# Kernel tuning notes

Hardware: AMD Instinct MI355X
Metric: run time of the kernel (lower is better)

The kernel has to match this reference:

```python
import jax, jax.numpy as jnp
import numpy as np

B, S, D, H = 2, 1024, 1024, 16
DH = D // H
EPS = 1e-5

def _ln(x, g, b):
    m = jnp.mean(x, axis=-1, keepdims=True)
    v = jnp.mean((x - m) ** 2, axis=-1, keepdims=True)
    return (x - m) / jnp.sqrt(v + EPS) * g + b

def setup_inputs() -> dict:
    key = jax.random.key(0)
    ks = jax.random.split(key, 5)
    scale = 1.0 / np.sqrt(D)
    return {
        "id": jax.random.normal(ks[0], (B, S, D), dtype=jnp.float32),
        "Wq": jax.random.uniform(ks[1], (D, D), jnp.float32, -scale, scale),
        "Wk": jax.random.uniform(ks[2], (D, D), jnp.float32, -scale, scale),
        "Wv": jax.random.uniform(ks[3], (D, D), jnp.float32, -scale, scale),
        "g0": jnp.ones((D,), jnp.float32), "b0": jnp.zeros((D,), jnp.float32),
        "g1": jnp.ones((D,), jnp.float32), "b1": jnp.zeros((D,), jnp.float32),
        "g2": jnp.ones((D,), jnp.float32), "b2": jnp.zeros((D,), jnp.float32),
    }

def reference(id, Wq, Wk, Wv, g0, b0, g1, b1, g2, b2):
    residual = id
    id_ln = _ln(id, g0, b0)
    # torch Linear: x @ W.T ; split heads along last dim, cat along batch
    q = (id_ln @ Wq.T).reshape(B, S, H, DH)
    k = (id_ln @ Wk.T).reshape(B, S, H, DH)
    v = (id_ln @ Wv.T).reshape(B, S, H, DH)
    scores = jnp.einsum('bqhd,bkhd->bhqk', q, k) / np.sqrt(DH)
    A = jax.nn.softmax(scores, axis=-1)                      # [B,H,S,S]
    O = jnp.einsum('bhqk,bkhd->bqhd', A, v).reshape(B, S, D)  # merge heads
    left = _ln(id_ln + O, g1, b1)
    right = _ln(residual + O, g2, b2)
    out = left + right
    # torch layout of A is [(H*B), S, S] with head-major ordering
    A_out = jnp.transpose(A, (1, 0, 2, 3)).reshape(H * B, S, S)
    return (out, A_out)
```

## Files before the change

### kernel.cpp

```cpp
#include <hip/hip_runtime.h>

namespace {

constexpr int B = 2, S = 1024, D = 1024, H = 16, DH = 64;
constexpr int M = B * S;
constexpr float EPS = 1e-5f;

using bf16x8 = __attribute__((ext_vector_type(8))) short;
using f32x4  = __attribute__((ext_vector_type(4))) float;

typedef const __attribute__((address_space(1))) void* gptr_t;
typedef __attribute__((address_space(3))) void* lptr_t;

__device__ __forceinline__ unsigned short f2bf(float f) {
    union { float f; unsigned u; } v{f};
    unsigned r = v.u + 0x7fffu + ((v.u >> 16) & 1u);
    return (unsigned short)(r >> 16);
}

__device__ __forceinline__ float wave_sum(float v) {
#pragma unroll
    for (int off = 32; off > 0; off >>= 1) v += __shfl_down(v, off, 64);
    return v;
}

__global__ __launch_bounds__(256) void cvt_w_kernel(
    const float* __restrict__ Wq, const float* __restrict__ Wk,
    const float* __restrict__ Wv, unsigned short* __restrict__ Wb)
{
    const float* src = (blockIdx.z == 0) ? Wq : (blockIdx.z == 1) ? Wk : Wv;
    const size_t i = ((size_t)blockIdx.x * 256 + threadIdx.x) * 4;
    float4 f = *reinterpret_cast<const float4*>(src + i);
    ushort4 h;
    h.x = f2bf(f.x); h.y = f2bf(f.y); h.z = f2bf(f.z); h.w = f2bf(f.w);
    *reinterpret_cast<ushort4*>(Wb + (size_t)blockIdx.z * D * D + i) = h;
}

__global__ __launch_bounds__(256) void ln0_kernel(
    const float* __restrict__ x, const float* __restrict__ g,
    const float* __restrict__ bt, float* __restrict__ y,
    unsigned short* __restrict__ yb)
{
    __shared__ float sm[8];
    __shared__ float stats[2];
    const int row = blockIdx.x;
    const int t = threadIdx.x;
    const float4 v = reinterpret_cast<const float4*>(x + (size_t)row * D)[t];
    float s  = v.x + v.y + v.z + v.w;
    float ss = v.x*v.x + v.y*v.y + v.z*v.z + v.w*v.w;
    s = wave_sum(s); ss = wave_sum(ss);
    const int lane = t & 63, wid = t >> 6;
    if (lane == 0) { sm[wid] = s; sm[4 + wid] = ss; }
    __syncthreads();
    if (t == 0) {
        float S1 = sm[0] + sm[1] + sm[2] + sm[3];
        float S2 = sm[4] + sm[5] + sm[6] + sm[7];
        float m  = S1 * (1.0f / D);
        float var = S2 * (1.0f / D) - m * m;
        stats[0] = m; stats[1] = rsqrtf(var + EPS);
    }
    __syncthreads();
    const float m = stats[0], r = stats[1];
    const float4 gv = reinterpret_cast<const float4*>(g)[t];
    const float4 bv = reinterpret_cast<const float4*>(bt)[t];
    float4 o;
    o.x = (v.x - m) * r * gv.x + bv.x;
    o.y = (v.y - m) * r * gv.y + bv.y;
    o.z = (v.z - m) * r * gv.z + bv.z;
    o.w = (v.w - m) * r * gv.w + bv.w;
    reinterpret_cast<float4*>(y + (size_t)row * D)[t] = o;
    ushort4 h; h.x = f2bf(o.x); h.y = f2bf(o.y); h.z = f2bf(o.z); h.w = f2bf(o.w);
    *reinterpret_cast<ushort4*>(yb + (size_t)row * D + t * 4) = h;
}

__global__ __launch_bounds__(256) void qkv_mfma_kernel(
    const unsigned short* __restrict__ idln, const unsigned short* __restrict__ Wb,
    unsigned short* __restrict__ q, unsigned short* __restrict__ k,
    unsigned short* __restrict__ vT)
{
    __shared__ unsigned short As[128 * 32];
    __shared__ unsigned short Bs[128 * 32];
    const int zi = blockIdx.z;
    const unsigned short* Bmat = Wb + (size_t)zi * D * D;
    const int m0 = blockIdx.y * 128, n0 = blockIdx.x * 128;
    const int t = threadIdx.x;
    const int w = t >> 6, lane = t & 63;
    const int wm = (w >> 1) * 64, wn = (w & 1) * 64;
    const int quad = lane >> 4, l16 = lane & 15;
    const int srow = t >> 2;
    const int scol = (t & 3) * 8;

    f32x4 acc[4][4];
#pragma unroll
    for (int i = 0; i < 4; ++i)
#pragma unroll
        for (int j = 0; j < 4; ++j) acc[i][j] = (f32x4){0.f, 0.f, 0.f, 0.f};

    for (int k0 = 0; k0 < D; k0 += 32) {
        __syncthreads();
#pragma unroll
        for (int c = 0; c < 2; ++c) {
            const unsigned short* ga = idln + (size_t)(m0 + srow + c * 64) * D + k0 + scol;
            __builtin_amdgcn_global_load_lds((gptr_t)ga, (lptr_t)(As + t * 8 + c * 2048), 16, 0, 0);
            const unsigned short* gb = Bmat + (size_t)(n0 + srow + c * 64) * D + k0 + scol;
            __builtin_amdgcn_global_load_lds((gptr_t)gb, (lptr_t)(Bs + t * 8 + c * 2048), 16, 0, 0);
        }
        __syncthreads();
        bf16x8 af[4], bfr[4];
#pragma unroll
        for (int i = 0; i < 4; ++i)
            af[i] = *reinterpret_cast<const bf16x8*>(As + (wm + i * 16 + l16) * 32 + quad * 8);
#pragma unroll
        for (int j = 0; j < 4; ++j)
            bfr[j] = *reinterpret_cast<const bf16x8*>(Bs + (wn + j * 16 + l16) * 32 + quad * 8);
#pragma unroll
        for (int i = 0; i < 4; ++i)
#pragma unroll
            for (int j = 0; j < 4; ++j)
                acc[i][j] = __builtin_amdgcn_mfma_f32_16x16x32_bf16(af[i], bfr[j], acc[i][j], 0, 0, 0);
    }

    if (zi < 2) {
        unsigned short* C = (zi == 0) ? q : k;
#pragma unroll
        for (int i = 0; i < 4; ++i)
#pragma unroll
            for (int j = 0; j < 4; ++j) {
                const int gcol = n0 + wn + j * 16 + l16;
#pragma unroll
                for (int reg = 0; reg < 4; ++reg) {
                    const int grow = m0 + wm + i * 16 + quad * 4 + reg;
                    C[(size_t)grow * D + gcol] = f2bf(acc[i][j][reg]);
                }
            }
    } else {
        const int b = m0 >> 10;
#pragma unroll
        for (int i = 0; i < 4; ++i)
#pragma unroll
            for (int j = 0; j < 4; ++j) {
                const int gcol = n0 + wn + j * 16 + l16;
                const int srow0 = (m0 - b * S) + wm + i * 16 + quad * 4;
                ushort4 h;
                h.x = f2bf(acc[i][j][0]); h.y = f2bf(acc[i][j][1]);
                h.z = f2bf(acc[i][j][2]); h.w = f2bf(acc[i][j][3]);
                *reinterpret_cast<ushort4*>(vT + ((size_t)b * D + gcol) * S + srow0) = h;
            }
    }
}

__global__ __launch_bounds__(256) void attn_fused_kernel(
    const unsigned short* __restrict__ q, const unsigned short* __restrict__ k,
    const unsigned short* __restrict__ vT, float* __restrict__ Aout,
    float* __restrict__ O)
{
    __shared__ unsigned short Qs[2 * 64 * 32];
    __shared__ unsigned short Ks[2 * 128 * 32];
    __shared__ unsigned short Vs[4 * 64 * 32];
    __shared__ unsigned short Ps[4 * 64 * 32];
    __shared__ float rs[4][64];
    __shared__ float sInv[64];

    const int z = blockIdx.z;
    const int b = z & 1, h = z >> 1;
    const int m0 = blockIdx.y * 64;
    const int t = threadIdx.x;
    const int w = t >> 6, lane = t & 63;
    const int quad = lane >> 4, l16 = lane & 15;
    const int wn = w * 32;
    const int sr = t >> 2, sc8 = (t & 3) * 8;

#pragma unroll
    for (int c = 0; c < 2; ++c) {
        const unsigned short* gq = q + (size_t)(b * S + m0 + sr) * D + h * DH + c * 32 + sc8;
        __builtin_amdgcn_global_load_lds((gptr_t)gq, (lptr_t)(Qs + c * 2048 + t * 8), 16, 0, 0);
    }

    float part[4][4];
#pragma unroll
    for (int i = 0; i < 4; ++i)
#pragma unroll
        for (int r = 0; r < 4; ++r) part[i][r] = 0.f;

    for (int n0 = 0; n0 < S; n0 += 128) {
        __syncthreads();
#pragma unroll
        for (int c = 0; c < 2; ++c)
#pragma unroll
            for (int cc = 0; cc < 2; ++cc) {
                const unsigned short* gk = k + (size_t)(b * S + n0 + cc * 64 + sr) * D + h * DH + c * 32 + sc8;
                __builtin_amdgcn_global_load_lds((gptr_t)gk, (lptr_t)(Ks + c * 4096 + cc * 2048 + t * 8), 16, 0, 0);
            }
        __syncthreads();
        f32x4 acc[4][2];
#pragma unroll
        for (int i = 0; i < 4; ++i)
#pragma unroll
            for (int j = 0; j < 2; ++j) acc[i][j] = (f32x4){0.f, 0.f, 0.f, 0.f};
#pragma unroll
        for (int c = 0; c < 2; ++c) {
            bf16x8 af[4], bfr[2];
#pragma unroll
            for (int i = 0; i < 4; ++i)
                af[i] = *reinterpret_cast<const bf16x8*>(Qs + c * 2048 + (i * 16 + l16) * 32 + quad * 8);
#pragma unroll
            for (int j = 0; j < 2; ++j)
                bfr[j] = *reinterpret_cast<const bf16x8*>(Ks + c * 4096 + (wn + j * 16 + l16) * 32 + quad * 8);
#pragma unroll
            for (int i = 0; i < 4; ++i)
#pragma unroll
                for (int j = 0; j < 2; ++j)
                    acc[i][j] = __builtin_amdgcn_mfma_f32_16x16x32_bf16(af[i], bfr[j], acc[i][j], 0, 0, 0);
        }
#pragma unroll
        for (int i = 0; i < 4; ++i)
#pragma unroll
            for (int j = 0; j < 2; ++j)
#pragma unroll
                for (int r = 0; r < 4; ++r)
                    part[i][r] += __expf(acc[i][j][r] * 0.125f);
    }
#pragma unroll
    for (int i = 0; i < 4; ++i)
#pragma unroll
        for (int r = 0; r < 4; ++r) {
            float p = part[i][r];
#pragma unroll
            for (int off = 1; off < 16; off <<= 1) p += __shfl_xor(p, off, 64);
            if (l16 == 0) rs[w][i * 16 + quad * 4 + r] = p;
        }
    __syncthreads();
    if (t < 64) sInv[t] = 1.0f / (rs[0][t] + rs[1][t] + rs[2][t] + rs[3][t]);

    float* Az = Aout + (size_t)z * S * S;
    f32x4 accO[4];
#pragma unroll
    for (int j = 0; j < 4; ++j) accO[j] = (f32x4){0.f, 0.f, 0.f, 0.f};

    for (int n0 = 0; n0 < S; n0 += 128) {
        __syncthreads();
#pragma unroll
        for (int c = 0; c < 2; ++c)
#pragma unroll
            for (int cc = 0; cc < 2; ++cc) {
                const unsigned short* gk = k + (size_t)(b * S + n0 + cc * 64 + sr) * D + h * DH + c * 32 + sc8;
                __builtin_amdgcn_global_load_lds((gptr_t)gk, (lptr_t)(Ks + c * 4096 + cc * 2048 + t * 8), 16, 0, 0);
            }
#pragma unroll
        for (int ks = 0; ks < 4; ++ks) {
            const unsigned short* gv = vT + ((size_t)b * D + h * DH + sr) * S + n0 + ks * 32 + sc8;
            __builtin_amdgcn_global_load_lds((gptr_t)gv, (lptr_t)(Vs + ks * 2048 + t * 8), 16, 0, 0);
        }
        __syncthreads();
        f32x4 acc[4][2];
#pragma unroll
        for (int i = 0; i < 4; ++i)
#pragma unroll
            for (int j = 0; j < 2; ++j) acc[i][j] = (f32x4){0.f, 0.f, 0.f, 0.f};
#pragma unroll
        for (int c = 0; c < 2; ++c) {
            bf16x8 af[4], bfr[2];
#pragma unroll
            for (int i = 0; i < 4; ++i)
                af[i] = *reinterpret_cast<const bf16x8*>(Qs + c * 2048 + (i * 16 + l16) * 32 + quad * 8);
#pragma unroll
            for (int j = 0; j < 2; ++j)
                bfr[j] = *reinterpret_cast<const bf16x8*>(Ks + c * 4096 + (wn + j * 16 + l16) * 32 + quad * 8);
#pragma unroll
            for (int i = 0; i < 4; ++i)
#pragma unroll
                for (int j = 0; j < 2; ++j)
                    acc[i][j] = __builtin_amdgcn_mfma_f32_16x16x32_bf16(af[i], bfr[j], acc[i][j], 0, 0, 0);
        }
#pragma unroll
        for (int i = 0; i < 4; ++i)
#pragma unroll
            for (int j = 0; j < 2; ++j)
#pragma unroll
                for (int r = 0; r < 4; ++r) {
                    const int rl = i * 16 + quad * 4 + r;
                    float a = __expf(acc[i][j][r] * 0.125f) * sInv[rl];
                    Az[(size_t)(m0 + rl) * S + n0 + wn + j * 16 + l16] = a;
                    Ps[w * 2048 + rl * 32 + j * 16 + l16] = f2bf(a);
                }
        __syncthreads();
#pragma unroll
        for (int ks = 0; ks < 4; ++ks) {
            bf16x8 af = *reinterpret_cast<const bf16x8*>(Ps + ks * 2048 + (w * 16 + l16) * 32 + quad * 8);
#pragma unroll
            for (int j = 0; j < 4; ++j) {
                bf16x8 bfr = *reinterpret_cast<const bf16x8*>(Vs + ks * 2048 + (j * 16 + l16) * 32 + quad * 8);
                accO[j] = __builtin_amdgcn_mfma_f32_16x16x32_bf16(af, bfr, accO[j], 0, 0, 0);
            }
        }
    }
#pragma unroll
    for (int j = 0; j < 4; ++j)
#pragma unroll
        for (int r = 0; r < 4; ++r) {
            const int grow = b * S + m0 + w * 16 + quad * 4 + r;
            O[(size_t)grow * D + h * DH + j * 16 + l16] = accO[j][r];
        }
}

__global__ __launch_bounds__(256) void final_kernel(
    const float* __restrict__ id, const float* __restrict__ id_ln, const float* __restrict__ O,
    const float* __restrict__ g1, const float* __restrict__ b1,
    const float* __restrict__ g2, const float* __restrict__ b2,
    float* __restrict__ out)
{
    __shared__ float sm[16];
    __shared__ float stats[4];
    const int row = blockIdx.x;
    const int t = threadIdx.x;
    const size_t base = (size_t)row * D;
    const float4 xi = reinterpret_cast<const float4*>(id + base)[t];
    const float4 xl = reinterpret_cast<const float4*>(id_ln + base)[t];
    const float4 xo = reinterpret_cast<const float4*>(O + base)[t];
    float4 t1, t2;
    t1.x = xl.x + xo.x; t1.y = xl.y + xo.y; t1.z = xl.z + xo.z; t1.w = xl.w + xo.w;
    t2.x = xi.x + xo.x; t2.y = xi.y + xo.y; t2.z = xi.z + xo.z; t2.w = xi.w + xo.w;
    float s1  = t1.x + t1.y + t1.z + t1.w;
    float ss1 = t1.x*t1.x + t1.y*t1.y + t1.z*t1.z + t1.w*t1.w;
    float s2  = t2.x + t2.y + t2.z + t2.w;
    float ss2 = t2.x*t2.x + t2.y*t2.y + t2.z*t2.z + t2.w*t2.w;
    s1 = wave_sum(s1); ss1 = wave_sum(ss1);
    s2 = wave_sum(s2); ss2 = wave_sum(ss2);
    const int lane = t & 63, wid = t >> 6;
    if (lane == 0) { sm[wid] = s1; sm[4+wid] = ss1; sm[8+wid] = s2; sm[12+wid] = ss2; }
    __syncthreads();
    if (t == 0) {
        float S1 = sm[0]+sm[1]+sm[2]+sm[3];
        float Q1 = sm[4]+sm[5]+sm[6]+sm[7];
        float S2 = sm[8]+sm[9]+sm[10]+sm[11];
        float Q2 = sm[12]+sm[13]+sm[14]+sm[15];
        float m1 = S1 * (1.0f / D);
        float m2 = S2 * (1.0f / D);
        stats[0] = m1; stats[1] = rsqrtf(Q1 * (1.0f / D) - m1*m1 + EPS);
        stats[2] = m2; stats[3] = rsqrtf(Q2 * (1.0f / D) - m2*m2 + EPS);
    }
    __syncthreads();
    const float m1 = stats[0], r1 = stats[1], m2 = stats[2], r2 = stats[3];
    const float4 g1v = reinterpret_cast<const float4*>(g1)[t];
    const float4 b1v = reinterpret_cast<const float4*>(b1)[t];
    const float4 g2v = reinterpret_cast<const float4*>(g2)[t];
    const float4 b2v = reinterpret_cast<const float4*>(b2)[t];
    float4 o;
    o.x = (t1.x - m1)*r1*g1v.x + b1v.x + (t2.x - m2)*r2*g2v.x + b2v.x;
    o.y = (t1.y - m1)*r1*g1v.y + b1v.y + (t2.y - m2)*r2*g2v.y + b2v.y;
    o.z = (t1.z - m1)*r1*g1v.z + b1v.z + (t2.z - m2)*r2*g2v.z + b2v.z;
    o.w = (t1.w - m1)*r1*g1v.w + b1v.w + (t2.w - m2)*r2*g2v.w + b2v.w;
    reinterpret_cast<float4*>(out + base)[t] = o;
}

}

extern "C" void kernel_launch(void* const* d_in, const int* in_sizes, int n_in,
                              void* d_out, int out_size, void* d_ws, size_t ws_size,
                              hipStream_t stream)
{
    const float* id = (const float*)d_in[0];
    const float* Wq = (const float*)d_in[1];
    const float* Wk = (const float*)d_in[2];
    const float* Wv = (const float*)d_in[3];
    const float* g0 = (const float*)d_in[4];
    const float* b0 = (const float*)d_in[5];
    const float* g1 = (const float*)d_in[6];
    const float* b1 = (const float*)d_in[7];
    const float* g2 = (const float*)d_in[8];
    const float* b2 = (const float*)d_in[9];

    float* out  = (float*)d_out;
    float* Aout = out + (size_t)B * S * D;

    char* ws = (char*)d_ws;
    float* id_ln  = (float*)(ws);
    float* O      = (float*)(ws + (8u << 20));
    unsigned short* idln_bf = (unsigned short*)(ws + (16u << 20));
    unsigned short* Wb      = idln_bf + (size_t)M * D;
    unsigned short* qb      = Wb + (size_t)3 * D * D;
    unsigned short* kb      = qb + (size_t)M * D;
    unsigned short* vT      = kb + (size_t)M * D;

    hipLaunchKernelGGL(cvt_w_kernel, dim3(D * D / 1024, 1, 3), dim3(256), 0, stream,
                       Wq, Wk, Wv, Wb);
    hipLaunchKernelGGL(ln0_kernel, dim3(M), dim3(256), 0, stream, id, g0, b0, id_ln, idln_bf);
    hipLaunchKernelGGL(qkv_mfma_kernel, dim3(D / 128, M / 128, 3), dim3(256), 0, stream,
                       idln_bf, Wb, qb, kb, vT);
    hipLaunchKernelGGL(attn_fused_kernel, dim3(1, S / 64, H * B), dim3(256), 0, stream,
                       qb, kb, vT, Aout, O);
    hipLaunchKernelGGL(final_kernel, dim3(M), dim3(256), 0, stream,
                       id, id_ln, O, g1, b1, g2, b2, out);
}
```

Baseline: 233.3 us.

## Restructure attention so each wave owns query rows and keeps P in registers

The attention kernel now has each wave own 16 query rows. It computes S^T via MFMA with K as the A operand, so the row sums stay in-lane and no cross-wave LDS reduction is needed. The probabilities feed the PV MFMA (16x16x16) straight from registers instead of going through a shared-memory P buffer, which removes a barrier per tile. A is now written as float4 vector stores, and the K/V tiles are narrowed to 64 keys per tile. In exchange there are more loop iterations with two barriers each, and it relies on the smaller-K bf16 MFMA.

```diff
diff --git a/kernel.cpp b/kernel.cpp
--- a/kernel.cpp
+++ b/kernel.cpp
@@ -7,6 +7,7 @@
 constexpr float EPS = 1e-5f;
 
 using bf16x8 = __attribute__((ext_vector_type(8))) short;
+using bf16x4 = __attribute__((ext_vector_type(4))) short;
 using f32x4  = __attribute__((ext_vector_type(4))) float;
 
 typedef const __attribute__((address_space(1))) void* gptr_t;
@@ -155,10 +156,8 @@
     float* __restrict__ O)
 {
     __shared__ unsigned short Qs[2 * 64 * 32];
-    __shared__ unsigned short Ks[2 * 128 * 32];
-    __shared__ unsigned short Vs[4 * 64 * 32];
-    __shared__ unsigned short Ps[4 * 64 * 32];
-    __shared__ float rs[4][64];
+    __shared__ unsigned short Ks[2 * 64 * 32];
+    __shared__ unsigned short Vs[4 * 64 * 16];
     __shared__ float sInv[64];
 
     const int z = blockIdx.z;
@@ -167,7 +166,6 @@
     const int t = threadIdx.x;
     const int w = t >> 6, lane = t & 63;
     const int quad = lane >> 4, l16 = lane & 15;
-    const int wn = w * 32;
     const int sr = t >> 2, sc8 = (t & 3) * 8;
 
 #pragma unroll
@@ -175,131 +173,89 @@
         const unsigned short* gq = q + (size_t)(b * S + m0 + sr) * D + h * DH + c * 32 + sc8;
         __builtin_amdgcn_global_load_lds((gptr_t)gq, (lptr_t)(Qs + c * 2048 + t * 8), 16, 0, 0);
     }
-
-    float part[4][4];
-#pragma unroll
-    for (int i = 0; i < 4; ++i)
-#pragma unroll
-        for (int r = 0; r < 4; ++r) part[i][r] = 0.f;
-
-    for (int n0 = 0; n0 < S; n0 += 128) {
-        __syncthreads();
-#pragma unroll
-        for (int c = 0; c < 2; ++c)
-#pragma unroll
-            for (int cc = 0; cc < 2; ++cc) {
-                const unsigned short* gk = k + (size_t)(b * S + n0 + cc * 64 + sr) * D + h * DH + c * 32 + sc8;
-                __builtin_amdgcn_global_load_lds((gptr_t)gk, (lptr_t)(Ks + c * 4096 + cc * 2048 + t * 8), 16, 0, 0);
-            }
-        __syncthreads();
-        f32x4 acc[4][2];
-#pragma unroll
-        for (int i = 0; i < 4; ++i)
-#pragma unroll
-            for (int j = 0; j < 2; ++j) acc[i][j] = (f32x4){0.f, 0.f, 0.f, 0.f};
+    __syncthreads();
+    bf16x8 qf[2];
+#pragma unroll
+    for (int c = 0; c < 2; ++c)
+        qf[c] = *reinterpret_cast<const bf16x8*>(Qs + c * 2048 + (w * 16 + l16) * 32 + quad * 8);
+
+    float rsum = 0.f;
+    for (int n0 = 0; n0 < S; n0 += 64) {
+        __syncthreads();
 #pragma unroll
         for (int c = 0; c < 2; ++c) {
-            bf16x8 af[4], bfr[2];
-#pragma unroll
-            for (int i = 0; i < 4; ++i)
-                af[i] = *reinterpret_cast<const bf16x8*>(Qs + c * 2048 + (i * 16 + l16) * 32 + quad * 8);
-#pragma unroll
-            for (int j = 0; j < 2; ++j)
-                bfr[j] = *reinterpret_cast<const bf16x8*>(Ks + c * 4096 + (wn + j * 16 + l16) * 32 + quad * 8);
-#pragma unroll
-            for (int i = 0; i < 4; ++i)
-#pragma unroll
-                for (int j = 0; j < 2; ++j)
-                    acc[i][j] = __builtin_amdgcn_mfma_f32_16x16x32_bf16(af[i], bfr[j], acc[i][j], 0, 0, 0);
-        }
-#pragma unroll
-        for (int i = 0; i < 4; ++i)
-#pragma unroll
-            for (int j = 0; j < 2; ++j)
-#pragma unroll
-                for (int r = 0; r < 4; ++r)
-                    part[i][r] += __expf(acc[i][j][r] * 0.125f);
-    }
-#pragma unroll
-    for (int i = 0; i < 4; ++i)
-#pragma unroll
-        for (int r = 0; r < 4; ++r) {
-            float p = part[i][r];
-#pragma unroll
-            for (int off = 1; off < 16; off <<= 1) p += __shfl_xor(p, off, 64);
-            if (l16 == 0) rs[w][i * 16 + quad * 4 + r] = p;
-        }
-    __syncthreads();
-    if (t < 64) sInv[t] = 1.0f / (rs[0][t] + rs[1][t] + rs[2][t] + rs[3][t]);
-
-    float* Az = Aout + (size_t)z * S * S;
+            const unsigned short* gk = k + (size_t)(b * S + n0 + sr) * D + h * DH + c * 32 + sc8;
+            __builtin_amdgcn_global_load_lds((gptr_t)gk, (lptr_t)(Ks + c * 2048 + t * 8), 16, 0, 0);
+        }
+        __syncthreads();
+#pragma unroll
+        for (int kt = 0; kt < 4; ++kt) {
+            f32x4 a = (f32x4){0.f, 0.f, 0.f, 0.f};
+#pragma unroll
+            for (int c = 0; c < 2; ++c) {
+                bf16x8 kf = *reinterpret_cast<const bf16x8*>(Ks + c * 2048 + (kt * 16 + l16) * 32 + quad * 8);
+                a = __builtin_amdgcn_mfma_f32_16x16x32_bf16(kf, qf[c], a, 0, 0, 0);
+            }
+#pragma unroll
+            for (int r = 0; r < 4; ++r) rsum += __expf(a[r] * 0.125f);
+        }
+    }
+    rsum += __shfl_xor(rsum, 16, 64);
+    rsum += __shfl_xor(rsum, 32, 64);
+    if (lane < 16) sInv[w * 16 + lane] = 1.0f / rsum;
+    const float sL = 1.0f / rsum;
+
     f32x4 accO[4];
 #pragma unroll
-    for (int j = 0; j < 4; ++j) accO[j] = (f32x4){0.f, 0.f, 0.f, 0.f};
-
-    for (int n0 = 0; n0 < S; n0 += 128) {
-        __syncthreads();
-#pragma unroll
-        for (int c = 0; c < 2; ++c)
-#pragma unroll
-            for (int cc = 0; cc < 2; ++cc) {
-                const unsigned short* gk = k + (size_t)(b * S + n0 + cc * 64 + sr) * D + h * DH + c * 32 + sc8;
-                __builtin_amdgcn_global_load_lds((gptr_t)gk, (lptr_t)(Ks + c * 4096 + cc * 2048 + t * 8), 16, 0, 0);
-            }
-#pragma unroll
-        for (int ks = 0; ks < 4; ++ks) {
-            const unsigned short* gv = vT + ((size_t)b * D + h * DH + sr) * S + n0 + ks * 32 + sc8;
-            __builtin_amdgcn_global_load_lds((gptr_t)gv, (lptr_t)(Vs + ks * 2048 + t * 8), 16, 0, 0);
-        }
-        __syncthreads();
-        f32x4 acc[4][2];
-#pragma unroll
-        for (int i = 0; i < 4; ++i)
-#pragma unroll
-            for (int j = 0; j < 2; ++j) acc[i][j] = (f32x4){0.f, 0.f, 0.f, 0.f};
+    for (int jj = 0; jj < 4; ++jj) accO[jj] = (f32x4){0.f, 0.f, 0.f, 0.f};
+
+    float* Az = Aout + (size_t)z * S * S + (size_t)(m0 + w * 16 + l16) * S;
+
+    for (int n0 = 0; n0 < S; n0 += 64) {
+        __syncthreads();
 #pragma unroll
         for (int c = 0; c < 2; ++c) {
-            bf16x8 af[4], bfr[2];
-#pragma unroll
-            for (int i = 0; i < 4; ++i)
-                af[i] = *reinterpret_cast<const bf16x8*>(Qs + c * 2048 + (i * 16 + l16) * 32 + quad * 8);
-#pragma unroll
-            for (int j = 0; j < 2; ++j)
-                bfr[j] = *reinterpret_cast<const bf16x8*>(Ks + c * 4096 + (wn + j * 16 + l16) * 32 + quad * 8);
-#pragma unroll
-            for (int i = 0; i < 4; ++i)
-#pragma unroll
-                for (int j = 0; j < 2; ++j)
-                    acc[i][j] = __builtin_amdgcn_mfma_f32_16x16x32_bf16(af[i], bfr[j], acc[i][j], 0, 0, 0);
-        }
-#pragma unroll
-        for (int i = 0; i < 4; ++i)
-#pragma unroll
-            for (int j = 0; j < 2; ++j)
-#pragma unroll
-                for (int r = 0; r < 4; ++r) {
-                    const int rl = i * 16 + quad * 4 + r;
-                    float a = __expf(acc[i][j][r] * 0.125f) * sInv[rl];
-                    Az[(size_t)(m0 + rl) * S + n0 + wn + j * 16 + l16] = a;
-                    Ps[w * 2048 + rl * 32 + j * 16 + l16] = f2bf(a);
-                }
-        __syncthreads();
-#pragma unroll
-        for (int ks = 0; ks < 4; ++ks) {
-            bf16x8 af = *reinterpret_cast<const bf16x8*>(Ps + ks * 2048 + (w * 16 + l16) * 32 + quad * 8);
-#pragma unroll
-            for (int j = 0; j < 4; ++j) {
-                bf16x8 bfr = *reinterpret_cast<const bf16x8*>(Vs + ks * 2048 + (j * 16 + l16) * 32 + quad * 8);
-                accO[j] = __builtin_amdgcn_mfma_f32_16x16x32_bf16(af, bfr, accO[j], 0, 0, 0);
-            }
-        }
-    }
-#pragma unroll
-    for (int j = 0; j < 4; ++j)
+            const unsigned short* gk = k + (size_t)(b * S + n0 + sr) * D + h * DH + c * 32 + sc8;
+            __builtin_amdgcn_global_load_lds((gptr_t)gk, (lptr_t)(Ks + c * 2048 + t * 8), 16, 0, 0);
+        }
+#pragma unroll
+        for (int c2 = 0; c2 < 2; ++c2) {
+            const int kt = c2 * 2 + (t >> 7);
+            const int dh = (t >> 1) & 63;
+            const int kh = t & 1;
+            const unsigned short* gv = vT + ((size_t)b * D + h * DH + dh) * S + n0 + kt * 16 + kh * 8;
+            __builtin_amdgcn_global_load_lds((gptr_t)gv, (lptr_t)(Vs + c2 * 2048 + t * 8), 16, 0, 0);
+        }
+        __syncthreads();
+#pragma unroll
+        for (int kt = 0; kt < 4; ++kt) {
+            f32x4 a = (f32x4){0.f, 0.f, 0.f, 0.f};
+#pragma unroll
+            for (int c = 0; c < 2; ++c) {
+                bf16x8 kf = *reinterpret_cast<const bf16x8*>(Ks + c * 2048 + (kt * 16 + l16) * 32 + quad * 8);
+                a = __builtin_amdgcn_mfma_f32_16x16x32_bf16(kf, qf[c], a, 0, 0, 0);
+            }
+            float e0 = __expf(a[0] * 0.125f) * sL;
+            float e1 = __expf(a[1] * 0.125f) * sL;
+            float e2 = __expf(a[2] * 0.125f) * sL;
+            float e3 = __expf(a[3] * 0.125f) * sL;
+            *reinterpret_cast<float4*>(Az + n0 + kt * 16 + quad * 4) = make_float4(e0, e1, e2, e3);
+            bf16x4 p;
+            p[0] = (short)f2bf(e0); p[1] = (short)f2bf(e1);
+            p[2] = (short)f2bf(e2); p[3] = (short)f2bf(e3);
+#pragma unroll
+            for (int jj = 0; jj < 4; ++jj) {
+                bf16x4 vv = *reinterpret_cast<const bf16x4*>(Vs + kt * 1024 + (jj * 16 + l16) * 16 + quad * 4);
+                accO[jj] = __builtin_amdgcn_mfma_f32_16x16x16bf16_1k(p, vv, accO[jj], 0, 0, 0);
+            }
+        }
+    }
+#pragma unroll
+    for (int jj = 0; jj < 4; ++jj)
 #pragma unroll
         for (int r = 0; r < 4; ++r) {
             const int grow = b * S + m0 + w * 16 + quad * 4 + r;
-            O[(size_t)grow * D + h * DH + j * 16 + l16] = accO[j][r];
+            O[(size_t)grow * D + h * DH + jj * 16 + l16] = accO[jj][r];
         }
 }
 
```

New measurement: 233.0 us. About the same (-0.1%).
